# Kernel tuning notes

Measured on AMD Instinct MI355X. Metric: run time of the kernel, lower is better.

The kernel has to match this reference:

```python
import jax, jax.numpy as jnp
import numpy as np

LAYERS = 20
STACKS = 2
LPS = LAYERS // STACKS  # layers per stack -> dilations 2**(l % LPS)
OUT_CH = 256
RES_CH = 64
GATE_CH = 128
SKIP_CH = 256


def setup_inputs() -> dict:
    key = jax.random.key(0)
    ks = jax.random.split(key, 16)
    B, T = 8, 16000
    s = 0.05
    inp = {
        "x": jax.random.normal(ks[0], (B, OUT_CH, T), dtype=jnp.float32),
        # first causal conv (note: original code applies w_pre to the shifted
        # input twice -> output is 2*w_pre(pre); w_cur is unused, so omitted)
        "w_pre0": jax.random.normal(ks[1], (RES_CH, OUT_CH)) * s,
        "b_pre0": jax.random.normal(ks[2], (RES_CH,)) * s,
        # per-layer dilated conv (no bias), residual block, skip projection
        "w_dil_pre": jax.random.normal(ks[3], (LAYERS, GATE_CH, RES_CH)) * s,
        "w_dil_cur": jax.random.normal(ks[4], (LAYERS, GATE_CH, RES_CH)) * s,
        "bias_h": jax.random.normal(ks[5], (LAYERS, GATE_CH)) * s,
        "w_res": jax.random.normal(ks[6], (LAYERS, RES_CH, RES_CH)) * s,
        "b_res": jax.random.normal(ks[7], (LAYERS, RES_CH)) * s,
        "w_skip": jax.random.normal(ks[8], (LAYERS, SKIP_CH, RES_CH)) * s,
        "b_skip": jax.random.normal(ks[9], (LAYERS, SKIP_CH)) * s,
        # output head
        "w_relu": jax.random.normal(ks[10], (SKIP_CH, SKIP_CH)) * s,
        "b_relu": jax.random.normal(ks[11], (SKIP_CH,)) * s,
        "w_out": jax.random.normal(ks[12], (OUT_CH, SKIP_CH)) * s,
        "b_out": jax.random.normal(ks[13], (OUT_CH,)) * s,
    }
    return inp


def _shift_right(h, d):
    # causal shift: pad d zeros on the left along time, drop last d samples
    return jnp.pad(h, ((0, 0), (0, 0), (d, 0)))[:, :, :-d]


def reference(x, w_pre0, b_pre0, w_dil_pre, w_dil_cur, bias_h,
              w_res, b_res, w_skip, b_skip, w_relu, b_relu, w_out, b_out):
    # first causal conv: original Conv2X1 'casual' path computes
    # w_pre(pre) + w_pre(pre) = 2 * w_pre(pre)  (faithful to source)
    pre = _shift_right(x, 1)
    h = 2.0 * (jnp.einsum('rc,bct->brt', w_pre0, pre) + b_pre0[None, :, None])

    skip = jnp.zeros((x.shape[0], SKIP_CH, x.shape[2]), dtype=h.dtype)
    for l in range(LAYERS):
        d = 2 ** (l % LPS)
        h_pre = _shift_right(h, d)
        # dilated 2x1 conv = two channel-wise linears (no bias), summed with bias_h
        a = (jnp.einsum('gr,brt->bgt', w_dil_pre[l], h_pre)
             + jnp.einsum('gr,brt->bgt', w_dil_cur[l], h)
             + bias_h[l][None, :, None])
        g = jnp.tanh(a[:, :RES_CH]) * jax.nn.sigmoid(a[:, RES_CH:])
        res = jnp.einsum('rq,bqt->brt', w_res[l], g) + b_res[l][None, :, None]
        h = h + res
        skip = skip + jnp.einsum('sr,brt->bst', w_skip[l], g) + b_skip[l][None, :, None]

    o = jax.nn.relu(skip)
    o = jnp.einsum('ps,bst->bpt', w_relu, o) + b_relu[None, :, None]
    o = jax.nn.relu(o)
    logits = jnp.einsum('os,bst->bot', w_out, o) + b_out[None, :, None]
    return jax.nn.softmax(logits, axis=1)  # (B, out_channels, T)
```

## Files before the change

kernel.cpp:

```cpp
#include <hip/hip_runtime.h>
#include <math.h>

#define B_ 8
#define T_ 16000
#define NBT 250
#define HROWS 16512
#define NLAY 20

typedef __attribute__((ext_vector_type(8))) short bf16x8;
typedef __attribute__((ext_vector_type(4))) float f32x4;
typedef __attribute__((ext_vector_type(4))) short sh4;

__device__ __forceinline__ unsigned short f2bf(float f){
  unsigned u = __float_as_uint(f);
  u += 0x7fffu + ((u >> 16) & 1u);
  return (unsigned short)(u >> 16);
}
__device__ __forceinline__ float bf2f(unsigned short s){
  return __uint_as_float(((unsigned)s) << 16);
}
__device__ __forceinline__ void split2(float v, unsigned short& hi, unsigned short& lo){
  hi = f2bf(v);
  lo = f2bf(v - bf2f(hi));
}

#define MFMA(a,b,c) __builtin_amdgcn_mfma_f32_16x16x32_bf16((a),(b),(c),0,0,0)

__device__ __forceinline__ void gload16(const short* gsrc, short* ldst){
  __builtin_amdgcn_global_load_lds(
      (const __attribute__((address_space(1))) unsigned int*)gsrc,
      (__attribute__((address_space(3))) unsigned int*)ldst, 16, 0, 0);
}

__global__ void k_split(const float* __restrict__ src, short* __restrict__ hi,
                        short* __restrict__ lo, int n){
  int idx = blockIdx.x * 256 + threadIdx.x;
  if (idx < n){
    unsigned short h, l; split2(src[idx], h, l);
    hi[idx] = (short)h; lo[idx] = (short)l;
  }
}
__global__ void k_split_gate(const float* __restrict__ wdp, const float* __restrict__ wdc,
                             short* __restrict__ hi, short* __restrict__ lo){
  int idx = blockIdx.x * 256 + threadIdx.x;
  if (idx < NLAY*128*128){
    int l   = idx >> 14;
    int rem = idx & 16383;
    int row = rem >> 7;
    int k   = rem & 127;
    float v = (k < 64) ? wdp[(l*128 + row)*64 + k] : wdc[(l*128 + row)*64 + (k-64)];
    unsigned short h, lo16; split2(v, h, lo16);
    hi[idx] = (short)h; lo[idx] = (short)lo16;
  }
}
__global__ void k_pack_wsf(const float* __restrict__ wsk, short* __restrict__ wsf){
  int idx = blockIdx.x * 256 + threadIdx.x;
  if (idx < NLAY*8*2*2*64*8){
    int e    = idx & 7;
    int j    = (idx >> 3) & 63;
    int kb2  = (idx >> 9) & 1;
    int half = (idx >> 10) & 1;
    int w    = (idx >> 11) & 7;
    int l    = idx >> 14;
    int row  = w*32 + half*16 + (j & 15);
    int ch   = (kb2*4 + (j >> 4))*8 + e;
    wsf[idx] = (short)f2bf(wsk[((size_t)l*256 + row)*64 + ch]);
  }
}
__global__ void k_bsum(const float* __restrict__ bsk, float* __restrict__ bsum){
  int s = threadIdx.x;
  if (s < 256){
    float a = 0.f;
#pragma unroll
    for (int l = 0; l < NLAY; ++l) a += bsk[l*256 + s];
    bsum[s] = a;
  }
}
__global__ void k_zero_guard(short* __restrict__ hA, short* __restrict__ hB){
  int idx = blockIdx.x * 256 + threadIdx.x;
  if (idx < B_*512*128){
    int b = idx / (512*128);
    int rem = idx - b*(512*128);
    size_t off = (size_t)b*HROWS*128 + rem;
    hA[off] = 0; hB[off] = 0;
  }
}

__global__ __launch_bounds__(512) void k_head_in(
    const float* __restrict__ x, const short* __restrict__ wph,
    const short* __restrict__ wpl, const float* __restrict__ bias,
    short* __restrict__ h)
{
  __shared__ short SXh[64*256], SXl[64*256];
  const int tid = threadIdx.x;
  const int bb = blockIdx.x / NBT;
  const int t0 = (blockIdx.x % NBT) * 64;
  const int lane = tid & 63, w = tid >> 6;
  const int l16 = lane & 15, l4 = lane >> 4;

  const float* xb = x + (size_t)bb * 256 * T_;
  {
    int col = lane;
    int t = t0 + col - 1;
#pragma unroll
    for (int p = 0; p < 16; ++p){
      int k0 = w*32 + p*2;
      float v0 = (t >= 0) ? xb[(size_t)k0*T_ + t] : 0.f;
      float v1 = (t >= 0) ? xb[(size_t)(k0+1)*T_ + t] : 0.f;
      unsigned short h0,l0,h1,l1; split2(v0,h0,l0); split2(v1,h1,l1);
      int idx = col*256 + (k0 ^ ((col & 15) << 3));
      ((unsigned int*)SXh)[idx>>1] = (unsigned)h0 | ((unsigned)h1 << 16);
      ((unsigned int*)SXl)[idx>>1] = (unsigned)l0 | ((unsigned)l1 << 16);
    }
  }
  __syncthreads();

  const int mi = w & 3, nh = w >> 2;
  const int rowA = mi*16 + l16;
  const int rt0 = mi*16 + l4*4;
  bf16x8 Ah[8], Al[8];
#pragma unroll
  for (int kb = 0; kb < 8; ++kb){
    int ko = kb*32 + l4*8;
    Ah[kb] = *(const bf16x8*)(wph + (size_t)rowA*256 + ko);
    Al[kb] = *(const bf16x8*)(wpl + (size_t)rowA*256 + ko);
  }
  short* hb = h + ((size_t)bb*HROWS + 512)*128;
#pragma unroll
  for (int nt = 0; nt < 2; ++nt){
    int col = (nh*2 + nt)*16 + l16;
    f32x4 acc = {0.f,0.f,0.f,0.f};
#pragma unroll
    for (int kb = 0; kb < 8; ++kb){
      int ko = (kb*32 + l4*8) ^ (l16 << 3);
      bf16x8 bhv = *(const bf16x8*)&SXh[col*256 + ko];
      bf16x8 blv = *(const bf16x8*)&SXl[col*256 + ko];
      acc = MFMA(Ah[kb], bhv, acc);
      acc = MFMA(Ah[kb], blv, acc);
      acc = MFMA(Al[kb], bhv, acc);
    }
    int t = t0 + col;
    int key = t & 15;
    int c  = rt0 >> 3, sub = rt0 & 7;
    sh4 hv, lv;
#pragma unroll
    for (int r = 0; r < 4; ++r){
      float v = 2.f*(acc[r] + bias[rt0 + r]);
      unsigned short hh, ll; split2(v, hh, ll);
      hv[r] = (short)hh; lv[r] = (short)ll;
    }
    *(sh4*)&hb[(size_t)t*128 + ((c ^ key) << 3) + sub] = hv;
    *(sh4*)&hb[(size_t)t*128 + (((c + 8) ^ key) << 3) + sub] = lv;
  }
}

__global__ __launch_bounds__(512) void k_layer4(
    const short* __restrict__ hin, short* __restrict__ hout,
    short* __restrict__ gout,
    const short* __restrict__ wgh, const short* __restrict__ wgl,
    const short* __restrict__ wrh, const short* __restrict__ wrlo,
    const float* __restrict__ bh, const float* __restrict__ br, int d)
{
  __shared__ short SH[64*128];
  __shared__ short SHP[64*128];
  __shared__ short SGh[64*64], SGl[64*64];
  const int tid = threadIdx.x;
  const int bb = blockIdx.x / NBT;
  const int tile = blockIdx.x % NBT;
  const int t0 = tile * 64;
  const int lane = tid & 63, w = tid >> 6;
  const int l16 = lane & 15, l4 = lane >> 4;

  const short* hb = hin + ((size_t)bb*HROWS + 512)*128;
  {
#pragma unroll
    for (int i = 0; i < 2; ++i){
      int colb = (w*2 + i)*4;
      const short* s1 = hb + (size_t)(t0 + colb + (lane>>4))*128 + (lane&15)*8;
      gload16(s1, &SH[colb*128]);
      const short* s2 = hb + (size_t)(t0 - d + colb + (lane>>4))*128 + (lane&15)*8;
      gload16(s2, &SHP[colb*128]);
    }
  }

  const int mi = w & 3, nh = w >> 2;
  const int rt0 = mi*16 + l4*4;
  const int rowt = mi*16 + l16, rows = 64 + mi*16 + l16;
  bf16x8 Ath[4], Atl[4], Ash[4], Asl[4];
#pragma unroll
  for (int kb = 0; kb < 4; ++kb){
    int ko = kb*32 + l4*8;
    Ath[kb] = *(const bf16x8*)(wgh + (size_t)rowt*128 + ko);
    Atl[kb] = *(const bf16x8*)(wgl + (size_t)rowt*128 + ko);
    Ash[kb] = *(const bf16x8*)(wgh + (size_t)rows*128 + ko);
    Asl[kb] = *(const bf16x8*)(wgl + (size_t)rows*128 + ko);
  }
  float bt[4], bs[4];
#pragma unroll
  for (int r = 0; r < 4; ++r){ bt[r] = bh[rt0+r]; bs[r] = bh[64+rt0+r]; }
  __syncthreads();

#pragma unroll
  for (int nt = 0; nt < 2; ++nt){
    int col = (nh*2 + nt)*16 + l16;
    int keyC = col & 15;
    int keyP = (col - d) & 15;
    f32x4 at = {0.f,0.f,0.f,0.f}, as = {0.f,0.f,0.f,0.f};
#pragma unroll
    for (int kb = 0; kb < 4; ++kb){
      const short* tile_p = (kb < 2) ? SHP : SH;
      int key = (kb < 2) ? keyP : keyC;
      int cb = (kb & 1)*4 + l4;
      bf16x8 bhv = *(const bf16x8*)&tile_p[col*128 + ((cb ^ key) << 3)];
      bf16x8 blv = *(const bf16x8*)&tile_p[col*128 + (((cb + 8) ^ key) << 3)];
      at = MFMA(Ath[kb], bhv, at);
      at = MFMA(Ath[kb], blv, at);
      at = MFMA(Atl[kb], bhv, at);
      as = MFMA(Ash[kb], bhv, as);
      as = MFMA(Ash[kb], blv, as);
      as = MFMA(Asl[kb], bhv, as);
    }
    unsigned short gh4[4], gl4[4];
#pragma unroll
    for (int r = 0; r < 4; ++r){
      float av = at[r] + bt[r];
      float sv = as[r] + bs[r];
      float e2 = __expf(2.f*av);
      float tv = 1.f - 2.f/(e2 + 1.f);
      float sg = 1.f/(1.f + __expf(-sv));
      float g  = tv*sg;
      split2(g, gh4[r], gl4[r]);
      int gi = col*64 + ((rt0 + r) ^ ((col & 7) << 3));
      SGh[gi] = (short)gh4[r]; SGl[gi] = (short)gl4[r];
    }
  }
  __syncthreads();

  {
    int f = tid >> 6, j = tid & 63;
    int row = (f >> 1)*16 + (j & 15);
    int c   = (f & 1)*4 + (j >> 4);
    bf16x8 v = *(const bf16x8*)&SGh[row*64 + ((c ^ (row & 7)) << 3)];
    *(bf16x8*)(gout + ((size_t)bb*NBT + tile)*4096 + tid*8) = v;
  }

  {
    const int rowA = mi*16 + l16;
    bf16x8 Rh[2], Rl[2];
#pragma unroll
    for (int kb = 0; kb < 2; ++kb){
      int ko = kb*32 + l4*8;
      Rh[kb] = *(const bf16x8*)(wrh  + (size_t)rowA*64 + ko);
      Rl[kb] = *(const bf16x8*)(wrlo + (size_t)rowA*64 + ko);
    }
    short* ho = hout + ((size_t)bb*HROWS + 512)*128;
    const int cH = rt0 >> 3, sub = rt0 & 7;
#pragma unroll
    for (int nt = 0; nt < 2; ++nt){
      int col = (nh*2 + nt)*16 + l16;
      int keyC = col & 15;
      f32x4 acc = {0.f,0.f,0.f,0.f};
#pragma unroll
      for (int kb = 0; kb < 2; ++kb){
        int ko = (kb*32 + l4*8) ^ ((col & 7) << 3);
        bf16x8 bhv = *(const bf16x8*)&SGh[col*64 + ko];
        bf16x8 blv = *(const bf16x8*)&SGl[col*64 + ko];
        acc = MFMA(Rh[kb], bhv, acc);
        acc = MFMA(Rh[kb], blv, acc);
        acc = MFMA(Rl[kb], bhv, acc);
      }
      sh4 hi4 = *(const sh4*)&SH[col*128 + ((cH ^ keyC) << 3) + sub];
      sh4 lo4 = *(const sh4*)&SH[col*128 + (((cH + 8) ^ keyC) << 3) + sub];
      int t = t0 + col;
      sh4 hv, lv;
#pragma unroll
      for (int r = 0; r < 4; ++r){
        float hin_f = bf2f((unsigned short)hi4[r]) + bf2f((unsigned short)lo4[r]);
        float v = hin_f + acc[r] + br[rt0 + r];
        unsigned short hh, ll; split2(v, hh, ll);
        hv[r] = (short)hh; lv[r] = (short)ll;
      }
      *(sh4*)&ho[(size_t)t*128 + ((cH ^ keyC) << 3) + sub] = hv;
      *(sh4*)&ho[(size_t)t*128 + (((cH + 8) ^ keyC) << 3) + sub] = lv;
    }
  }
}

__global__ __launch_bounds__(512) void k_head_fused(
    float* __restrict__ io,
    const short* __restrict__ g,
    const short* __restrict__ wsf,
    const float* __restrict__ bsum,
    const short* __restrict__ wrlh, const short* __restrict__ wrll,
    const float* __restrict__ brl,
    const short* __restrict__ woh, const short* __restrict__ wol,
    const float* __restrict__ bo)
{
  __shared__ short S1h[64*256];
  __shared__ float smax[8][64], ssum[8][64];
  const int tid = threadIdx.x;
  const int bb = blockIdx.x / NBT;
  const int tile = blockIdx.x % NBT;
  const int t0 = tile * 64;
  const int lane = tid & 63, w = tid >> 6;
  const int l16 = lane & 15, l4 = lane >> 4;

  const int r0 = w*32 + l16, r1 = w*32 + 16 + l16;
  const int rtb0 = w*32 + l4*4, rtb1 = rtb0 + 16;

  f32x4 acc0[4], acc1[4];
#pragma unroll
  for (int nt = 0; nt < 4; ++nt){ acc0[nt] = (f32x4){0.f,0.f,0.f,0.f}; acc1[nt] = (f32x4){0.f,0.f,0.f,0.f}; }

  {
    const size_t LSTR = (size_t)B_ * NBT * 4096;
    const short* gb = g + ((size_t)bb*NBT + tile)*4096 + lane*8;
    const short* wb = wsf + (size_t)w*2048 + lane*8;
    for (int l20 = 0; l20 < 20; ++l20){
      const short* gt = gb + (size_t)l20*LSTR;
      const short* wl = wb + (size_t)l20*16384;
      bf16x8 A00 = *(const bf16x8*)(wl);
      bf16x8 A01 = *(const bf16x8*)(wl + 512);
      bf16x8 A10 = *(const bf16x8*)(wl + 1024);
      bf16x8 A11 = *(const bf16x8*)(wl + 1536);
      bf16x8 Bv[4][2];
#pragma unroll
      for (int nt = 0; nt < 4; ++nt){
#pragma unroll
        for (int kb2 = 0; kb2 < 2; ++kb2)
          Bv[nt][kb2] = *(const bf16x8*)(gt + (nt*2 + kb2)*512);
      }
#pragma unroll
      for (int nt = 0; nt < 4; ++nt){
        acc0[nt] = MFMA(A00, Bv[nt][0], acc0[nt]);
        acc0[nt] = MFMA(A01, Bv[nt][1], acc0[nt]);
        acc1[nt] = MFMA(A10, Bv[nt][0], acc1[nt]);
        acc1[nt] = MFMA(A11, Bv[nt][1], acc1[nt]);
      }
    }
  }

  {
    float bs0[4], bs1[4];
#pragma unroll
    for (int r = 0; r < 4; ++r){ bs0[r] = bsum[rtb0+r]; bs1[r] = bsum[rtb1+r]; }
#pragma unroll
    for (int nt = 0; nt < 4; ++nt){
      int c2 = nt*16 + l16;
      unsigned short h[4];
#pragma unroll
      for (int r = 0; r < 4; ++r)
        h[r] = f2bf(fmaxf(acc0[nt][r] + bs0[r], 0.f));
      int i0 = c2*256 + (rtb0 ^ (l16 << 3));
      ((unsigned int*)&S1h[i0])[0] = (unsigned)h[0] | ((unsigned)h[1] << 16);
      ((unsigned int*)&S1h[i0])[1] = (unsigned)h[2] | ((unsigned)h[3] << 16);
#pragma unroll
      for (int r = 0; r < 4; ++r)
        h[r] = f2bf(fmaxf(acc1[nt][r] + bs1[r], 0.f));
      int i1 = c2*256 + (rtb1 ^ (l16 << 3));
      ((unsigned int*)&S1h[i1])[0] = (unsigned)h[0] | ((unsigned)h[1] << 16);
      ((unsigned int*)&S1h[i1])[1] = (unsigned)h[2] | ((unsigned)h[3] << 16);
    }
  }
  __syncthreads();

#pragma unroll
  for (int nt = 0; nt < 4; ++nt){ acc0[nt] = (f32x4){0.f,0.f,0.f,0.f}; acc1[nt] = (f32x4){0.f,0.f,0.f,0.f}; }
#pragma unroll
  for (int kb = 0; kb < 8; ++kb){
    int ko = kb*32 + l4*8;
    bf16x8 A0h = *(const bf16x8*)(wrlh + (size_t)r0*256 + ko);
    bf16x8 A0l = *(const bf16x8*)(wrll + (size_t)r0*256 + ko);
    bf16x8 A1h = *(const bf16x8*)(wrlh + (size_t)r1*256 + ko);
    bf16x8 A1l = *(const bf16x8*)(wrll + (size_t)r1*256 + ko);
#pragma unroll
    for (int nt = 0; nt < 4; ++nt){
      int c2 = nt*16 + l16;
      int kos = ko ^ (l16 << 3);
      bf16x8 bhv = *(const bf16x8*)&S1h[c2*256 + kos];
      acc0[nt] = MFMA(A0h, bhv, acc0[nt]);
      acc0[nt] = MFMA(A0l, bhv, acc0[nt]);
      acc1[nt] = MFMA(A1h, bhv, acc1[nt]);
      acc1[nt] = MFMA(A1l, bhv, acc1[nt]);
    }
  }
  __syncthreads();
  {
    float br0[4], br1[4];
#pragma unroll
    for (int r = 0; r < 4; ++r){ br0[r] = brl[rtb0+r]; br1[r] = brl[rtb1+r]; }
#pragma unroll
    for (int nt = 0; nt < 4; ++nt){
      int c2 = nt*16 + l16;
      unsigned short h[4];
#pragma unroll
      for (int r = 0; r < 4; ++r)
        h[r] = f2bf(fmaxf(acc0[nt][r] + br0[r], 0.f));
      int i0 = c2*256 + (rtb0 ^ (l16 << 3));
      ((unsigned int*)&S1h[i0])[0] = (unsigned)h[0] | ((unsigned)h[1] << 16);
      ((unsigned int*)&S1h[i0])[1] = (unsigned)h[2] | ((unsigned)h[3] << 16);
#pragma unroll
      for (int r = 0; r < 4; ++r)
        h[r] = f2bf(fmaxf(acc1[nt][r] + br1[r], 0.f));
      int i1 = c2*256 + (rtb1 ^ (l16 << 3));
      ((unsigned int*)&S1h[i1])[0] = (unsigned)h[0] | ((unsigned)h[1] << 16);
      ((unsigned int*)&S1h[i1])[1] = (unsigned)h[2] | ((unsigned)h[3] << 16);
    }
  }
  __syncthreads();

#pragma unroll
  for (int nt = 0; nt < 4; ++nt){ acc0[nt] = (f32x4){0.f,0.f,0.f,0.f}; acc1[nt] = (f32x4){0.f,0.f,0.f,0.f}; }
#pragma unroll
  for (int kb = 0; kb < 8; ++kb){
    int ko = kb*32 + l4*8;
    bf16x8 A0h = *(const bf16x8*)(woh + (size_t)r0*256 + ko);
    bf16x8 A0l = *(const bf16x8*)(wol + (size_t)r0*256 + ko);
    bf16x8 A1h = *(const bf16x8*)(woh + (size_t)r1*256 + ko);
    bf16x8 A1l = *(const bf16x8*)(wol + (size_t)r1*256 + ko);
#pragma unroll
    for (int nt = 0; nt < 4; ++nt){
      int c2 = nt*16 + l16;
      int kos = ko ^ (l16 << 3);
      bf16x8 bhv = *(const bf16x8*)&S1h[c2*256 + kos];
      acc0[nt] = MFMA(A0h, bhv, acc0[nt]);
      acc0[nt] = MFMA(A0l, bhv, acc0[nt]);
      acc1[nt] = MFMA(A1h, bhv, acc1[nt]);
      acc1[nt] = MFMA(A1l, bhv, acc1[nt]);
    }
  }
  float* iob = io + (size_t)bb * 256 * T_;
  float bo0[4], bo1[4];
#pragma unroll
  for (int r = 0; r < 4; ++r){ bo0[r] = bo[rtb0+r]; bo1[r] = bo[rtb1+r]; }
#pragma unroll
  for (int nt = 0; nt < 4; ++nt){
    float m = -1e30f;
#pragma unroll
    for (int r = 0; r < 4; ++r){
      acc0[nt][r] += bo0[r];
      acc1[nt][r] += bo1[r];
      m = fmaxf(m, fmaxf(acc0[nt][r], acc1[nt][r]));
    }
    m = fmaxf(m, __shfl_xor(m, 16, 64));
    m = fmaxf(m, __shfl_xor(m, 32, 64));
    smax[w][nt*16 + l16] = m;
  }
  __syncthreads();
#pragma unroll
  for (int nt = 0; nt < 4; ++nt){
    float m = smax[0][nt*16 + l16];
#pragma unroll
    for (int ww = 1; ww < 8; ++ww) m = fmaxf(m, smax[ww][nt*16 + l16]);
    float s = 0.f;
#pragma unroll
    for (int r = 0; r < 4; ++r){
      acc0[nt][r] = __expf(acc0[nt][r] - m); s += acc0[nt][r];
      acc1[nt][r] = __expf(acc1[nt][r] - m); s += acc1[nt][r];
    }
    s += __shfl_xor(s, 16, 64);
    s += __shfl_xor(s, 32, 64);
    ssum[w][nt*16 + l16] = s;
  }
  __syncthreads();
#pragma unroll
  for (int nt = 0; nt < 4; ++nt){
    float S = 0.f;
#pragma unroll
    for (int ww = 0; ww < 8; ++ww) S += ssum[ww][nt*16 + l16];
    float inv = 1.f / S;
    int t = t0 + nt*16 + l16;
#pragma unroll
    for (int r = 0; r < 4; ++r){
      iob[(size_t)(rtb0 + r)*T_ + t] = acc0[nt][r]*inv;
      iob[(size_t)(rtb1 + r)*T_ + t] = acc1[nt][r]*inv;
    }
  }
}

extern "C" void kernel_launch(void* const* d_in, const int* in_sizes, int n_in,
                              void* d_out, int out_size, void* d_ws, size_t ws_size,
                              hipStream_t stream) {
  const float* x       = (const float*)d_in[0];
  const float* w_pre0  = (const float*)d_in[1];
  const float* b_pre0  = (const float*)d_in[2];
  const float* w_dil_p = (const float*)d_in[3];
  const float* w_dil_c = (const float*)d_in[4];
  const float* bias_h  = (const float*)d_in[5];
  const float* w_res   = (const float*)d_in[6];
  const float* b_res   = (const float*)d_in[7];
  const float* w_skip  = (const float*)d_in[8];
  const float* b_skip  = (const float*)d_in[9];
  const float* w_relu  = (const float*)d_in[10];
  const float* b_relu  = (const float*)d_in[11];
  const float* w_out   = (const float*)d_in[12];
  const float* b_out   = (const float*)d_in[13];

  float* out = (float*)d_out;
  short* hA = (short*)d_ws;
  short* hB = hA + (size_t)B_ * HROWS * 128;
  float* bsum = (float*)(hB + (size_t)B_ * HROWS * 128);
  short* p   = (short*)(bsum + 256);
  short* WPh = p; p += 16384;  short* WPl = p; p += 16384;
  short* WGh = p; p += 327680; short* WGl = p; p += 327680;
  short* WRh = p; p += 81920;  short* WRl = p; p += 81920;
  short* WSF = p; p += 327680;
  short* WLh = p; p += 65536;  short* WLl = p; p += 65536;
  short* WOh = p; p += 65536;  short* WOl = p; p += 65536;
  short* GBUF = p;

  k_split<<<64, 256, 0, stream>>>(w_pre0, WPh, WPl, 16384);
  k_split_gate<<<1280, 256, 0, stream>>>(w_dil_p, w_dil_c, WGh, WGl);
  k_split<<<320, 256, 0, stream>>>(w_res, WRh, WRl, 81920);
  k_pack_wsf<<<1280, 256, 0, stream>>>(w_skip, WSF);
  k_split<<<256, 256, 0, stream>>>(w_relu, WLh, WLl, 65536);
  k_split<<<256, 256, 0, stream>>>(w_out, WOh, WOl, 65536);
  k_zero_guard<<<2048, 256, 0, stream>>>(hA, hB);
  k_bsum<<<1, 256, 0, stream>>>(b_skip, bsum);

  k_head_in<<<B_ * NBT, 512, 0, stream>>>(x, WPh, WPl, b_pre0, hA);

  const short* hin = hA;
  short* houtp = hB;
  for (int l = 0; l < NLAY; ++l) {
    int d = 1 << (l % 10);
    k_layer4<<<B_ * NBT, 512, 0, stream>>>(
        hin, houtp,
        GBUF + (size_t)l * B_ * NBT * 4096,
        WGh + (size_t)l*16384, WGl + (size_t)l*16384,
        WRh + (size_t)l*4096,  WRl + (size_t)l*4096,
        bias_h + (size_t)l*128, b_res + (size_t)l*64, d);
    const short* tmp = hin;
    hin = houtp;
    houtp = (short*)tmp;
  }

  k_head_fused<<<B_ * NBT, 512, 0, stream>>>(
      out, GBUF, WSF, bsum, WLh, WLl, b_relu, WOh, WOl, b_out);
}
```

Baseline: 1.468 ms.

## Double-buffer gate tiles through LDS in head skip-accumulation loop

The head kernel's per-layer loop now stages each layer's gate tile into a double-buffered LDS region with async loads, prefetching the next layer while computing the current one. Before, all 8 warps read the same gate tile redundantly from global memory. The softmax reduction scratch reuses the staging buffer to keep LDS usage flat. It adds a block barrier per layer iteration and depends on the gload16 helper's semantics.

```diff
diff --git a/kernel.cpp b/kernel.cpp
--- a/kernel.cpp
+++ b/kernel.cpp
@@ -296,8 +296,8 @@
     const short* __restrict__ woh, const short* __restrict__ wol,
     const float* __restrict__ bo)
 {
+  __shared__ short GT[2][64*64];
   __shared__ short S1h[64*256];
-  __shared__ float smax[8][64], ssum[8][64];
   const int tid = threadIdx.x;
   const int bb = blockIdx.x / NBT;
   const int tile = blockIdx.x % NBT;
@@ -314,30 +314,33 @@
 
   {
     const size_t LSTR = (size_t)B_ * NBT * 4096;
-    const short* gb = g + ((size_t)bb*NBT + tile)*4096 + lane*8;
+    const short* gtile = g + ((size_t)bb*NBT + tile)*4096;
     const short* wb = wsf + (size_t)w*2048 + lane*8;
+
+#define STAGE(l20, buf) gload16(gtile + (size_t)(l20)*LSTR + w*512 + lane*8, &GT[buf][w*512])
+
+    STAGE(0, 0);
+    __syncthreads();
     for (int l20 = 0; l20 < 20; ++l20){
-      const short* gt = gb + (size_t)l20*LSTR;
+      if (l20 + 1 < 20) STAGE(l20 + 1, (l20 + 1) & 1);
       const short* wl = wb + (size_t)l20*16384;
       bf16x8 A00 = *(const bf16x8*)(wl);
       bf16x8 A01 = *(const bf16x8*)(wl + 512);
       bf16x8 A10 = *(const bf16x8*)(wl + 1024);
       bf16x8 A11 = *(const bf16x8*)(wl + 1536);
-      bf16x8 Bv[4][2];
+      const short* gt = &GT[l20 & 1][0];
 #pragma unroll
       for (int nt = 0; nt < 4; ++nt){
-#pragma unroll
-        for (int kb2 = 0; kb2 < 2; ++kb2)
-          Bv[nt][kb2] = *(const bf16x8*)(gt + (nt*2 + kb2)*512);
+        bf16x8 B0 = *(const bf16x8*)(gt + (nt*2    )*512 + lane*8);
+        bf16x8 B1 = *(const bf16x8*)(gt + (nt*2 + 1)*512 + lane*8);
+        acc0[nt] = MFMA(A00, B0, acc0[nt]);
+        acc0[nt] = MFMA(A01, B1, acc0[nt]);
+        acc1[nt] = MFMA(A10, B0, acc1[nt]);
+        acc1[nt] = MFMA(A11, B1, acc1[nt]);
       }
-#pragma unroll
-      for (int nt = 0; nt < 4; ++nt){
-        acc0[nt] = MFMA(A00, Bv[nt][0], acc0[nt]);
-        acc0[nt] = MFMA(A01, Bv[nt][1], acc0[nt]);
-        acc1[nt] = MFMA(A10, Bv[nt][0], acc1[nt]);
-        acc1[nt] = MFMA(A11, Bv[nt][1], acc1[nt]);
-      }
-    }
+      __syncthreads();
+    }
+#undef STAGE
   }
 
   {
@@ -429,6 +432,8 @@
       acc1[nt] = MFMA(A1l, bhv, acc1[nt]);
     }
   }
+  float* smax = (float*)&GT[0][0];
+  float* ssum = smax + 512;
   float* iob = io + (size_t)bb * 256 * T_;
   float bo0[4], bo1[4];
 #pragma unroll
@@ -444,14 +449,14 @@
     }
     m = fmaxf(m, __shfl_xor(m, 16, 64));
     m = fmaxf(m, __shfl_xor(m, 32, 64));
-    smax[w][nt*16 + l16] = m;
+    smax[w*64 + nt*16 + l16] = m;
   }
   __syncthreads();
 #pragma unroll
   for (int nt = 0; nt < 4; ++nt){
-    float m = smax[0][nt*16 + l16];
-#pragma unroll
-    for (int ww = 1; ww < 8; ++ww) m = fmaxf(m, smax[ww][nt*16 + l16]);
+    float m = smax[nt*16 + l16];
+#pragma unroll
+    for (int ww = 1; ww < 8; ++ww) m = fmaxf(m, smax[ww*64 + nt*16 + l16]);
     float s = 0.f;
 #pragma unroll
     for (int r = 0; r < 4; ++r){
@@ -460,14 +465,14 @@
     }
     s += __shfl_xor(s, 16, 64);
     s += __shfl_xor(s, 32, 64);
-    ssum[w][nt*16 + l16] = s;
+    ssum[w*64 + nt*16 + l16] = s;
   }
   __syncthreads();
 #pragma unroll
   for (int nt = 0; nt < 4; ++nt){
     float S = 0.f;
 #pragma unroll
-    for (int ww = 0; ww < 8; ++ww) S += ssum[ww][nt*16 + l16];
+    for (int ww = 0; ww < 8; ++ww) S += ssum[ww*64 + nt*16 + l16];
     float inv = 1.f / S;
     int t = t0 + nt*16 + l16;
 #pragma unroll
```

After: 1.337 ms. 1.1x faster.
